# Kernel optimization log

Hardware: AMD Instinct MI355X
Metric: run time of the kernel (lower is better)

## Reference

```python
import jax, jax.numpy as jnp
import numpy as np

# Geometry constants matching __init__ defaults
DG = 2        # deformable_groups
KS = 3        # kernel_size
K = KS * KS   # taps per kernel
DIL = 2       # dilation
PAD = 2       # padding = dilation
STRIDE = 1


def setup_inputs() -> dict:
    key = jax.random.key(0)
    k1, k2, k3, k4 = jax.random.split(key, 4)
    B, C, H, W = 4, 128, 96, 192
    Cout = 128
    x = jax.random.normal(k1, (B, C, H, W), dtype=jnp.float32)
    # offset/mask conv: grouped conv, groups=DG -> in-channels per group = C//DG
    off_out = DG * 3 * K  # 54 (36 offset + 18 mask)
    # small weights so learned offsets are O(1) pixels (realistic trained regime;
    # the original zero-init would make the gather trivial)
    w_offset = jax.random.normal(k2, (off_out, C // DG, KS, KS), dtype=jnp.float32) * 0.01
    b_offset = jax.random.normal(k3, (off_out,), dtype=jnp.float32) * 0.1
    stdv = 1.0 / np.sqrt(C * KS * KS)
    w_deform = jax.random.uniform(k4, (Cout, C, KS, KS), dtype=jnp.float32,
                                  minval=-stdv, maxval=stdv)
    return {"x": x, "w_offset": w_offset, "b_offset": b_offset, "w_deform": w_deform}


def _deform_conv2d(x, w_offset, b_offset, w_deform):
    B, C, H, W = x.shape
    Cout = w_deform.shape[0]
    Cg = C // DG
    # --- offset/mask conv (grouped, dilated) ---
    om = jax.lax.conv_general_dilated(
        x, w_offset, (STRIDE, STRIDE), [(PAD, PAD), (PAD, PAD)],
        rhs_dilation=(DIL, DIL), feature_group_count=DG,
        dimension_numbers=("NCHW", "OIHW", "NCHW"))
    om = om + b_offset[None, :, None, None]
    Ho, Wo = om.shape[2], om.shape[3]
    off_ch = DG * 2 * K
    offset = om[:, :off_ch]                       # [B, 36, Ho, Wo]
    mask = jax.nn.sigmoid(om[:, off_ch:]) * 2.0   # double_mask=True -> *2
    # torchvision layout: channel 2*(g*K+k) = dy, +1 = dx
    off = offset.reshape(B, DG, K, 2, Ho, Wo)
    m = mask.reshape(B, DG, K, Ho, Wo)
    # --- sampling coordinates ---
    ky = (jnp.arange(K) // KS).astype(x.dtype)
    kx = (jnp.arange(K) % KS).astype(x.dtype)
    base_y = (jnp.arange(Ho) * STRIDE - PAD).astype(x.dtype)
    base_x = (jnp.arange(Wo) * STRIDE - PAD).astype(x.dtype)
    py = base_y[None, None, None, :, None] + (ky * DIL)[None, None, :, None, None] + off[:, :, :, 0]
    px = base_x[None, None, None, None, :] + (kx * DIL)[None, None, :, None, None] + off[:, :, :, 1]
    y0 = jnp.floor(py)
    x0 = jnp.floor(px)
    ty = py - y0
    tx = px - x0
    xflat = x.reshape(B, DG, Cg, H * W)
    # gather[b,g,c,n] = xflat[b,g,c, idx[b,g,n]]
    gather = jax.vmap(jax.vmap(lambda xg, idx: jnp.take(xg, idx, axis=1)))
    val = jnp.zeros((B, DG, Cg, K, Ho, Wo), x.dtype)
    # accumulate bilinear corners one at a time to bound peak memory
    for dy, dx, wgt in ((0, 0, (1 - ty) * (1 - tx)), (0, 1, (1 - ty) * tx),
                        (1, 0, ty * (1 - tx)), (1, 1, ty * tx)):
        yy = y0 + dy
        xx = x0 + dx
        valid = (yy >= 0) & (yy < H) & (xx >= 0) & (xx < W)
        yc = jnp.clip(yy, 0, H - 1).astype(jnp.int32)
        xc = jnp.clip(xx, 0, W - 1).astype(jnp.int32)
        lin = (yc * W + xc).reshape(B, DG, K * Ho * Wo)
        g = gather(xflat, lin).reshape(B, DG, Cg, K, Ho, Wo)
        val = val + jnp.where(valid, wgt, 0.0)[:, :, None] * g
    val = val * m[:, :, None]  # modulation mask per deformable group / tap
    wr = w_deform.reshape(Cout, DG, Cg, K)
    return jnp.einsum("ogck,bgckhw->bohw", wr, val)


def reference(x, w_offset, b_offset, w_deform):
    return _deform_conv2d(x, w_offset, b_offset, w_deform)
```

## Files before the change

### kernel.cpp

```cpp
#include <hip/hip_runtime.h>
#include <hip/hip_fp16.h>
#include <math.h>

#define BB   4
#define C_   128
#define H_   96
#define W_   192
#define COUT 128
#define DG_  2
#define CG_  64
#define K_   9
#define HO   96
#define WO   192
#define HW   (H_ * W_)
#define OMCH 54
#define RDIM (C_ * K_)
#define NKS  (RDIM / 32)
#define CSTEP 4
#define NCH  (NKS / CSTEP)
#define VROW 18

typedef __attribute__((ext_vector_type(8))) short bf16x8;
typedef __attribute__((ext_vector_type(8))) _Float16 f16x8;
typedef __attribute__((ext_vector_type(4))) float f32x4;

static __device__ __forceinline__ ushort f2bf(float f) {
  union { float f; uint u; } v; v.f = f;
  uint r = v.u + 0x7fff + ((v.u >> 16) & 1);
  return (ushort)(r >> 16);
}

__global__ __launch_bounds__(256) void prep_k(
    const float* __restrict__ wd, const float* __restrict__ wo,
    ushort* __restrict__ WtA, ushort* __restrict__ Awo) {
  int i = blockIdx.x * 256 + threadIdx.x;
  if (i < 128 * RDIM) {
    int blkA = i >> 9, within = i & 511;
    int oct = within >> 7, colA = (within >> 3) & 15, j = within & 7;
    int m = blkA & 1, wvq = (blkA >> 1) & 3, s = blkA >> 3;
    int o = wvq * 32 + m * 16 + colA;
    int r = s * 32 + oct * 8 + j;
    int g = r / 576, t = r - g * 576;
    int k = t >> 6, cg = t & 63;
    WtA[i] = __half_as_ushort(__float2half(wd[((size_t)o * C_ + g * 64 + cg) * 9 + k]));
  }
  if (i < 64 * RDIM) {
    int o2 = i / RDIM, r = i - o2 * RDIM;
    int k = r >> 7, c = r & 127;
    int g = o2 >> 5, j = o2 & 31;
    float v = (((c >> 6) == g) && (j < 27))
                ? wo[(((size_t)(g * 27 + j)) * 64 + (c & 63)) * 9 + k] : 0.f;
    Awo[i] = f2bf(v);
  }
}

__global__ __launch_bounds__(256) void xt_k(
    const float* __restrict__ x, __half* __restrict__ xT) {
  __shared__ float t[128][65];
  int blk = blockIdx.x;
  int b = blk / 288, p0 = (blk % 288) * 64;
  int q = threadIdx.x >> 6, l = threadIdx.x & 63;
  const float* xb = x + (size_t)b * C_ * HW;
#pragma unroll
  for (int it = 0; it < 32; ++it) {
    int c = q * 32 + it;
    t[c][l] = xb[(size_t)c * HW + p0 + l];
  }
  __syncthreads();
  uint* xTb = (uint*)(xT + (size_t)b * HW * 128);
#pragma unroll
  for (int it = 0; it < 16; ++it) {
    int px = q * 16 + it;
    union { __half2 h; uint u; } pk;
    pk.h = __half2{__float2half(t[2 * l][px]), __float2half(t[2 * l + 1][px])};
    xTb[(size_t)(p0 + px) * 64 + l] = pk.u;
  }
}

__global__ __launch_bounds__(256) void offset_mfma_k(
    const float* __restrict__ x, const ushort* __restrict__ Awo,
    const float* __restrict__ b_offset, float* __restrict__ om) {
  __shared__ uint s_val[2][64][20];

  int bid = blockIdx.x;
  int blk = (bid & 7) * 144 + (bid >> 3);
  int wt = blk % 3, bh = blk / 3;
  int ho = bh % HO, b = bh / HO;
  int wo0 = wt * 64;
  int lane = threadIdx.x & 63, wv = threadIdx.x >> 6;

  const float* xb = x + (size_t)b * C_ * HW;
  f32x4 acc[4];
#pragma unroll
  for (int n = 0; n < 4; ++n) acc[n] = (f32x4){0.f, 0.f, 0.f, 0.f};

  const ushort* abase = Awo + (size_t)(wv * 16 + (lane & 15)) * RDIM + (lane >> 4) * 8;

  float gv[8];

  auto patch_gather = [&](int step) {
    int k = step >> 2;
    int dy = k / 3, dx = k - dy * 3;
    int y  = ho - 2 + 2 * dy;
    int xc = wo0 + lane - 2 + 2 * dx;
    bool ok = (y >= 0) & (y < H_) & (xc >= 0) & (xc < W_);
    int c0 = (step & 3) * 32 + wv * 8;
    const float* pl = xb + ((ptrdiff_t)c0 * HW + y * W_ + xc);
#pragma unroll
    for (int j = 0; j < 8; ++j) { gv[j] = ok ? *pl : 0.f; pl += HW; }
  };

  auto patch_finish = [&](int nb) {
    uint res[4];
#pragma unroll
    for (int j = 0; j < 8; ++j) {
      uint bf = (uint)f2bf(gv[j]);
      if (j & 1) res[j >> 1] |= bf << 16; else res[j >> 1] = bf;
    }
    *(int4*)&s_val[nb][lane][wv * 4] = *(int4*)&res[0];
  };

  auto mfma_step = [&](int step, int cb) {
    bf16x8 af = *(const bf16x8*)(abase + step * 32);
#pragma unroll
    for (int n = 0; n < 4; ++n) {
      bf16x8 bfr = *(const bf16x8*)&s_val[cb][n * 16 + (lane & 15)][(lane >> 4) * 4];
      acc[n] = __builtin_amdgcn_mfma_f32_16x16x32_bf16(af, bfr, acc[n], 0, 0, 0);
    }
  };

  patch_gather(0);
  patch_finish(0);
  __syncthreads();
  for (int it = 0; it < NKS - 1; ++it) {
    patch_gather(it + 1);
    mfma_step(it, it & 1);
    patch_finish((it + 1) & 1);
    __syncthreads();
  }
  mfma_step(NKS - 1, (NKS - 1) & 1);

  int col = lane & 15, rgrp = lane >> 4;
#pragma unroll
  for (int n = 0; n < 4; ++n)
#pragma unroll
    for (int ri = 0; ri < 4; ++ri) {
      int o2 = wv * 16 + rgrp * 4 + ri;
      int g = o2 >> 5, j = o2 & 31;
      if (j < 27) {
        int ch = g * 27 + j;
        om[((size_t)(b * OMCH + ch) * HO + ho) * WO + wo0 + n * 16 + col] =
            acc[n][ri] + b_offset[ch];
      }
    }
}

__global__ __launch_bounds__(256, 3) void deform_main_k(
    const __half* __restrict__ xT, const float* __restrict__ om,
    const ushort* __restrict__ WtA, float* __restrict__ out) {
  __shared__ uint  s_addr[18 * 64];
  __shared__ uint2 s_wq[18 * 64];
  __shared__ uint  s_val[2][CSTEP * 64 * VROW];

  int bid = blockIdx.x;
  int blk = (bid & 7) * 144 + (bid >> 3);
  int wt = blk % 3, bh = blk / 3;
  int ho = bh % HO, b = bh / HO;
  int wo0 = wt * 64;
  int tid = threadIdx.x;
  int lane = tid & 63, wv = tid >> 6;

  for (int e = tid; e < 18 * 64; e += 256) {
    int px = e & 63, gk = e >> 6;
    int g = gk / 9, k = gk - g * 9;
    int wo = wo0 + px;
    const float* omb = om + (size_t)b * OMCH * HW + (size_t)ho * WO + wo;
    float offy = omb[(size_t)(g * 18 + k * 2 + 0) * HW];
    float offx = omb[(size_t)(g * 18 + k * 2 + 1) * HW];
    float z    = omb[(size_t)(36 + g * 9 + k) * HW];
    float msk  = 2.f / (1.f + __expf(-z));
    float py = (float)(ho - 2 + (k / 3) * 2) + offy;
    float px_ = (float)(wo - 2 + (k % 3) * 2) + offx;
    float y0f = floorf(py), x0f = floorf(px_);
    int   y0 = (int)y0f, x0 = (int)x0f;
    float ty = py - y0f, tx = px_ - x0f;
    float wy0 = (y0 >= 0 && y0 < H_)      ? (1.f - ty) : 0.f;
    float wy1 = (y0 >= -1 && y0 < H_ - 1) ? ty         : 0.f;
    float wx0 = (x0 >= 0 && x0 < W_)      ? (1.f - tx) : 0.f;
    float wx1 = (x0 >= -1 && x0 < W_ - 1) ? tx         : 0.f;
    int yb  = min(max(y0, 0), H_ - 2);
    int xb_ = min(max(x0, 0), W_ - 2);
    float wAy = (y0 == yb      ? wy0 : 0.f) + (y0 + 1 == yb      ? wy1 : 0.f);
    float wBy = (y0 == yb + 1  ? wy0 : 0.f) + (y0 + 1 == yb + 1  ? wy1 : 0.f);
    float wAx = (x0 == xb_     ? wx0 : 0.f) + (x0 + 1 == xb_     ? wx1 : 0.f);
    float wBx = (x0 == xb_ + 1 ? wx0 : 0.f) + (x0 + 1 == xb_ + 1 ? wx1 : 0.f);
    s_addr[e] = (uint)((yb * W_ + xb_) * 128);
    union { __half2 h; uint u; } uA, uB;
    uA.h = __half2{__float2half(wAy * wAx * msk), __float2half(wAy * wBx * msk)};
    uB.h = __half2{__float2half(wBy * wAx * msk), __float2half(wBy * wBx * msk)};
    s_wq[e] = make_uint2(uA.u, uB.u);
  }

  const __half* xTb = xT + (size_t)b * HW * 128;
  int sub = lane >> 3, q = lane & 7;
  int col = lane & 15, oct = lane >> 4;

  f32x4 acc[2][4];
#pragma unroll
  for (int m = 0; m < 2; ++m)
#pragma unroll
    for (int n = 0; n < 4; ++n) acc[m][n] = (f32x4){0.f, 0.f, 0.f, 0.f};

  uint4 C0[4], C1[4], C2[4], C3[4];
  uint2 WQ[4];
  int   IX[4];

  auto issue_chunk = [&](int c) {
#pragma unroll
    for (int t = 0; t < 4; ++t) {
      int idx = wv * 4 + t;
      int gkl = idx >> 3, po = idx & 7;
      int gk = c * 2 + gkl;
      int px = po * 8 + sub;
      int ci = gk * 64 + px;
      uint base = s_addr[ci];
      WQ[t] = s_wq[ci];
      int g = gk >= 9;
      const __half* p = xTb + base + g * 64 + q * 8;
      C0[t] = *(const uint4*)(p);
      C1[t] = *(const uint4*)(p + 128);
      C2[t] = *(const uint4*)(p + W_ * 128);
      C3[t] = *(const uint4*)(p + W_ * 128 + 128);
      int step_local = 2 * gkl + (q >> 2);
      int row = step_local * 64 + px;
      IX[t] = row * VROW + (q & 3) * 4;
    }
  };

  auto finish_chunk = [&](int nb) {
#pragma unroll
    for (int t = 0; t < 4; ++t) {
      union { __half2 h; uint u; } w0, w1;
      w0.u = WQ[t].x; w1.u = WQ[t].y;
      __half2 wAx = __low2half2(w0.h), wAy = __high2half2(w0.h);
      __half2 wBx = __low2half2(w1.h), wBy = __high2half2(w1.h);
      uint res[4];
      const uint* a  = (const uint*)&C0[t];
      const uint* b1 = (const uint*)&C1[t];
      const uint* c2 = (const uint*)&C2[t];
      const uint* d  = (const uint*)&C3[t];
#pragma unroll
      for (int h = 0; h < 4; ++h) {
        union { __half2 h2; uint u; } p0, p1, p2, p3, vv;
        p0.u = a[h]; p1.u = b1[h]; p2.u = c2[h]; p3.u = d[h];
        __half2 v = __hmul2(p0.h2, wAx);
        v = __hfma2(p1.h2, wAy, v);
        v = __hfma2(p2.h2, wBx, v);
        v = __hfma2(p3.h2, wBy, v);
        vv.h2 = v;
        res[h] = vv.u;
      }
      *(uint4*)&s_val[nb][IX[t]] = make_uint4(res[0], res[1], res[2], res[3]);
    }
  };

  auto mfma_chunk = [&](int c, int cb) {
#pragma unroll
    for (int ls = 0; ls < CSTEP; ++ls) {
      int s = c * CSTEP + ls;
      const ushort* ab = WtA + (size_t)((s * 4 + wv) * 2) * 512 + (oct * 16 + col) * 8;
      f16x8 a0 = *(const f16x8*)(ab);
      f16x8 a1 = *(const f16x8*)(ab + 512);
#pragma unroll
      for (int n = 0; n < 4; ++n) {
        f16x8 bfr = *(const f16x8*)
            &s_val[cb][(ls * 64 + n * 16 + col) * VROW + oct * 4];
        acc[0][n] = __builtin_amdgcn_mfma_f32_16x16x32_f16(a0, bfr, acc[0][n], 0, 0, 0);
        acc[1][n] = __builtin_amdgcn_mfma_f32_16x16x32_f16(a1, bfr, acc[1][n], 0, 0, 0);
      }
    }
  };

  __syncthreads();
  issue_chunk(0);
  finish_chunk(0);
  __syncthreads();

  for (int c = 0; c < NCH; ++c) {
    if (c < NCH - 1) issue_chunk(c + 1);
    mfma_chunk(c, c & 1);
    if (c < NCH - 1) finish_chunk((c + 1) & 1);
    __syncthreads();
  }

#pragma unroll
  for (int m = 0; m < 2; ++m)
#pragma unroll
    for (int n = 0; n < 4; ++n)
#pragma unroll
      for (int ri = 0; ri < 4; ++ri) {
        int o = wv * 32 + m * 16 + oct * 4 + ri;
        out[((size_t)(b * COUT + o) * HO + ho) * WO + wo0 + n * 16 + col] = acc[m][n][ri];
      }
}

extern "C" void kernel_launch(void* const* d_in, const int* in_sizes, int n_in,
                              void* d_out, int out_size, void* d_ws, size_t ws_size,
                              hipStream_t stream) {
  const float* x        = (const float*)d_in[0];
  const float* w_offset = (const float*)d_in[1];
  const float* b_offset = (const float*)d_in[2];
  const float* w_deform = (const float*)d_in[3];
  float* out = (float*)d_out;

  char* ws = (char*)d_ws;
  float*  om  = (float*)ws;
  ushort* WtA = (ushort*)(ws + 15925248);
  ushort* Awo = (ushort*)(ws + 15925248 + 294912);
  __half* xT  = (__half*)(ws + 15925248 + 294912 + 147456);

  prep_k<<<576, 256, 0, stream>>>(w_deform, w_offset, WtA, Awo);
  xt_k<<<1152, 256, 0, stream>>>(x, xT);
  offset_mfma_k<<<1152, 256, 0, stream>>>(x, Awo, b_offset, om);
  deform_main_k<<<1152, 256, 0, stream>>>(xT, om, WtA, out);
}
```

Baseline: 112.0 us.

## Rewrite offset conv to read channel-last fp16 input with chunked MFMA pipeline

The offset/mask convolution now reads the fp16 NHWC copy of x that the main kernel already uses, with 16-byte vector loads per pixel, instead of strided NCHW fp32 loads that had to be converted to bf16. The weights are repacked into an MFMA-tiled fp16 layout, and the work is processed in chunks of four k-steps with double-buffered LDS, which means fewer barriers. This is meant to cut uncoalesced global traffic and sync overhead. It creates a dependency on xt_k finishing first and switches the offset computation from bf16 to fp16 precision.

After: 92.05 us. 1.22x faster.

```diff
diff --git a/kernel.cpp b/kernel.cpp
--- a/kernel.cpp
+++ b/kernel.cpp
@@ -20,7 +20,6 @@
 #define NCH  (NKS / CSTEP)
 #define VROW 18
 
-typedef __attribute__((ext_vector_type(8))) short bf16x8;
 typedef __attribute__((ext_vector_type(8))) _Float16 f16x8;
 typedef __attribute__((ext_vector_type(4))) float f32x4;
 
@@ -32,7 +31,7 @@
 
 __global__ __launch_bounds__(256) void prep_k(
     const float* __restrict__ wd, const float* __restrict__ wo,
-    ushort* __restrict__ WtA, ushort* __restrict__ Awo) {
+    ushort* __restrict__ WtA, ushort* __restrict__ Awo2) {
   int i = blockIdx.x * 256 + threadIdx.x;
   if (i < 128 * RDIM) {
     int blkA = i >> 9, within = i & 511;
@@ -45,12 +44,17 @@
     WtA[i] = __half_as_ushort(__float2half(wd[((size_t)o * C_ + g * 64 + cg) * 9 + k]));
   }
   if (i < 64 * RDIM) {
-    int o2 = i / RDIM, r = i - o2 * RDIM;
-    int k = r >> 7, c = r & 127;
-    int g = o2 >> 5, j = o2 & 31;
-    float v = (((c >> 6) == g) && (j < 27))
-                ? wo[(((size_t)(g * 27 + j)) * 64 + (c & 63)) * 9 + k] : 0.f;
-    Awo[i] = f2bf(v);
+    int blkA = i >> 9, within = i & 511;
+    int oct = within >> 7, colA = (within >> 3) & 15, j = within & 7;
+    int wv2 = blkA & 3, s = blkA >> 2;
+    int o2 = wv2 * 16 + colA;
+    int r = s * 32 + oct * 8 + j;
+    int g = r / 576, t = r - g * 576;
+    int k = t >> 6, cg = t & 63;
+    int g2 = o2 >> 5, j2 = o2 & 31;
+    float v = ((g2 == g) && (j2 < 27))
+                ? wo[(((size_t)(g2 * 27 + j2)) * 64 + cg) * 9 + k] : 0.f;
+    Awo2[i] = __half_as_ushort(__float2half(v));
   }
 }
 
@@ -77,75 +81,101 @@
   }
 }
 
-__global__ __launch_bounds__(256) void offset_mfma_k(
-    const float* __restrict__ x, const ushort* __restrict__ Awo,
+__global__ __launch_bounds__(256, 4) void offset_nhwc_k(
+    const __half* __restrict__ xT, const ushort* __restrict__ Awo2,
     const float* __restrict__ b_offset, float* __restrict__ om) {
-  __shared__ uint s_val[2][64][20];
+  __shared__ uint s_val[2][CSTEP * 64 * VROW];
 
   int bid = blockIdx.x;
   int blk = (bid & 7) * 144 + (bid >> 3);
   int wt = blk % 3, bh = blk / 3;
   int ho = bh % HO, b = bh / HO;
   int wo0 = wt * 64;
-  int lane = threadIdx.x & 63, wv = threadIdx.x >> 6;
-
-  const float* xb = x + (size_t)b * C_ * HW;
+  int tid = threadIdx.x;
+  int lane = tid & 63, wv = tid >> 6;
+  int sub = lane >> 3, q = lane & 7;
+  int col = lane & 15, oct = lane >> 4;
+
+  const __half* xTb = xT + (size_t)b * HW * 128;
+
   f32x4 acc[4];
 #pragma unroll
   for (int n = 0; n < 4; ++n) acc[n] = (f32x4){0.f, 0.f, 0.f, 0.f};
 
-  const ushort* abase = Awo + (size_t)(wv * 16 + (lane & 15)) * RDIM + (lane >> 4) * 8;
-
-  float gv[8];
-
-  auto patch_gather = [&](int step) {
-    int k = step >> 2;
-    int dy = k / 3, dx = k - dy * 3;
-    int y  = ho - 2 + 2 * dy;
-    int xc = wo0 + lane - 2 + 2 * dx;
-    bool ok = (y >= 0) & (y < H_) & (xc >= 0) & (xc < W_);
-    int c0 = (step & 3) * 32 + wv * 8;
-    const float* pl = xb + ((ptrdiff_t)c0 * HW + y * W_ + xc);
-#pragma unroll
-    for (int j = 0; j < 8; ++j) { gv[j] = ok ? *pl : 0.f; pl += HW; }
-  };
-
-  auto patch_finish = [&](int nb) {
-    uint res[4];
-#pragma unroll
-    for (int j = 0; j < 8; ++j) {
-      uint bf = (uint)f2bf(gv[j]);
-      if (j & 1) res[j >> 1] |= bf << 16; else res[j >> 1] = bf;
-    }
-    *(int4*)&s_val[nb][lane][wv * 4] = *(int4*)&res[0];
-  };
-
-  auto mfma_step = [&](int step, int cb) {
-    bf16x8 af = *(const bf16x8*)(abase + step * 32);
-#pragma unroll
-    for (int n = 0; n < 4; ++n) {
-      bf16x8 bfr = *(const bf16x8*)&s_val[cb][n * 16 + (lane & 15)][(lane >> 4) * 4];
-      acc[n] = __builtin_amdgcn_mfma_f32_16x16x32_bf16(af, bfr, acc[n], 0, 0, 0);
-    }
-  };
-
-  patch_gather(0);
-  patch_finish(0);
+  uint4 C0[4];
+  uint  MK[4];
+  int   IX[4];
+
+  auto issue_chunk = [&](int c) {
+#pragma unroll
+    for (int t = 0; t < 4; ++t) {
+      int idx = wv * 4 + t;
+      int gkl = idx >> 3, po = idx & 7;
+      int gk = c * 2 + gkl;
+      int px = po * 8 + sub;
+      int g = gk >= 9, k = gk - 9 * g;
+      int dy = k / 3, dx = k - dy * 3;
+      int y  = ho - 2 + 2 * dy;
+      int xc = wo0 + px - 2 + 2 * dx;
+      bool ok = (y >= 0) & (y < H_) & (xc >= 0) & (xc < W_);
+      int yc  = min(max(y, 0), H_ - 1);
+      int xcc = min(max(xc, 0), W_ - 1);
+      const __half* p = xTb + (size_t)(yc * W_ + xcc) * 128 + g * 64 + q * 8;
+      C0[t] = *(const uint4*)(p);
+      MK[t] = ok ? 0x3c003c00u : 0u;
+      int step_local = 2 * gkl + (q >> 2);
+      IX[t] = (step_local * 64 + px) * VROW + (q & 3) * 4;
+    }
+  };
+
+  auto finish_chunk = [&](int nb) {
+#pragma unroll
+    for (int t = 0; t < 4; ++t) {
+      union { __half2 h2; uint u; } m; m.u = MK[t];
+      uint res[4];
+      const uint* a = (const uint*)&C0[t];
+#pragma unroll
+      for (int h = 0; h < 4; ++h) {
+        union { __half2 h2; uint u; } p, vv;
+        p.u = a[h];
+        vv.h2 = __hmul2(p.h2, m.h2);
+        res[h] = vv.u;
+      }
+      *(uint4*)&s_val[nb][IX[t]] = make_uint4(res[0], res[1], res[2], res[3]);
+    }
+  };
+
+  auto mfma_chunk = [&](int c, int cb) {
+#pragma unroll
+    for (int ls = 0; ls < CSTEP; ++ls) {
+      int s = c * CSTEP + ls;
+      const ushort* ab = Awo2 + (size_t)(s * 4 + wv) * 512 + (oct * 16 + col) * 8;
+      f16x8 a0 = *(const f16x8*)(ab);
+#pragma unroll
+      for (int n = 0; n < 4; ++n) {
+        f16x8 bfr = *(const f16x8*)
+            &s_val[cb][(ls * 64 + n * 16 + col) * VROW + oct * 4];
+        acc[n] = __builtin_amdgcn_mfma_f32_16x16x32_f16(a0, bfr, acc[n], 0, 0, 0);
+      }
+    }
+  };
+
+  issue_chunk(0);
+  finish_chunk(0);
   __syncthreads();
-  for (int it = 0; it < NKS - 1; ++it) {
-    patch_gather(it + 1);
-    mfma_step(it, it & 1);
-    patch_finish((it + 1) & 1);
+
+  for (int c = 0; c < NCH; ++c) {
+    if (c < NCH - 1) issue_chunk(c + 1);
+    mfma_chunk(c, c & 1);
+    if (c < NCH - 1) finish_chunk((c + 1) & 1);
     __syncthreads();
   }
-  mfma_step(NKS - 1, (NKS - 1) & 1);
-
-  int col = lane & 15, rgrp = lane >> 4;
+
 #pragma unroll
   for (int n = 0; n < 4; ++n)
 #pragma unroll
     for (int ri = 0; ri < 4; ++ri) {
-      int o2 = wv * 16 + rgrp * 4 + ri;
+      int o2 = wv * 16 + oct * 4 + ri;
       int g = o2 >> 5, j = o2 & 31;
       if (j < 27) {
         int ch = g * 27 + j;
@@ -314,13 +344,13 @@
   float* out = (float*)d_out;
 
   char* ws = (char*)d_ws;
-  float*  om  = (float*)ws;
-  ushort* WtA = (ushort*)(ws + 15925248);
-  ushort* Awo = (ushort*)(ws + 15925248 + 294912);
-  __half* xT  = (__half*)(ws + 15925248 + 294912 + 147456);
-
-  prep_k<<<576, 256, 0, stream>>>(w_deform, w_offset, WtA, Awo);
+  float*  om   = (float*)ws;
+  ushort* WtA  = (ushort*)(ws + 15925248);
+  ushort* Awo2 = (ushort*)(ws + 15925248 + 294912);
+  __half* xT   = (__half*)(ws + 15925248 + 294912 + 147456);
+
+  prep_k<<<576, 256, 0, stream>>>(w_deform, w_offset, WtA, Awo2);
   xt_k<<<1152, 256, 0, stream>>>(x, xT);
-  offset_mfma_k<<<1152, 256, 0, stream>>>(x, Awo, b_offset, om);
+  offset_nhwc_k<<<1152, 256, 0, stream>>>(xT, Awo2, b_offset, om);
   deform_main_k<<<1152, 256, 0, stream>>>(xT, om, WtA, out);
 }
```
